# Optimization experiments

Hardware: AMD Instinct MI355X
Metric: run time of the kernel (lower is better)

## Reference

```python
import jax, jax.numpy as jnp
import numpy as np

N_GRAPHS = 32
NUM_NODES = 2848
N = N_GRAPHS * NUM_NODES  # 91136
E = 1_000_000
K = 3   # num_stacks
T = 5   # num_layers
HID = 32
EPS = 1e-5


def setup_inputs() -> dict:
    key = jax.random.key(0)
    ks = jax.random.split(key, 32)
    s = 0.1
    rn = lambda k, shp: (jax.random.normal(k, shp, jnp.float32) * s)
    inp = {
        "x": jax.random.normal(ks[0], (N, 2), jnp.float32),
        "edge_index": jax.random.randint(ks[1], (2, E), 0, N, dtype=jnp.int32).astype(jnp.int64),
        "weights": jax.random.uniform(ks[2], (E,), jnp.float32),
        "batch": (jnp.arange(N) // NUM_NODES).astype(jnp.int64),
        # ARMAConv1: 2 -> 32
        "iw1": rn(ks[3], (K, 2, HID)),
        "w1": rn(ks[4], (T - 1, K, HID, HID)),
        "rw1": rn(ks[5], (T, K, 2, HID)),
        "b1": rn(ks[6], (T, K, 1, HID)),
        "g1": jnp.ones((HID,), jnp.float32), "be1": jnp.zeros((HID,), jnp.float32),
        # ARMAConv2: 32 -> 32
        "iw2": rn(ks[7], (K, HID, HID)),
        "w2": rn(ks[8], (T - 1, K, HID, HID)),
        "rw2": rn(ks[9], (T, K, HID, HID)),
        "b2": rn(ks[10], (T, K, 1, HID)),
        "g2": jnp.ones((HID,), jnp.float32), "be2": jnp.zeros((HID,), jnp.float32),
        # ARMAConv3: 32 -> 1
        "iw3": rn(ks[11], (K, HID, 1)),
        "w3": rn(ks[12], (T - 1, K, 1, 1)),
        "rw3": rn(ks[13], (T, K, HID, 1)),
        "b3": rn(ks[14], (T, K, 1, 1)),
        "g3": jnp.ones((1,), jnp.float32), "be3": jnp.zeros((1,), jnp.float32),
        # classifier Linear(1, 1)
        "cw": rn(ks[15], (1, 1)),
        "cb": jnp.zeros((1,), jnp.float32),
    }
    return inp


def gcn_norm(row, col, w, n):
    # deg over targets, sym normalization, no self loops (PyG ARMAConv default)
    deg = jnp.zeros((n,), w.dtype).at[col].add(w)
    dis = jnp.where(deg > 0, jax.lax.rsqrt(jnp.where(deg > 0, deg, 1.0)), 0.0)
    return dis[row] * w * dis[col]


def arma_conv(x, row, col, norm, iw, w, rw, b):
    # x: [N, Fin]; returns [N, Fout] (mean over K stacks)
    out = None
    for t in range(T):
        if t == 0:
            h = jnp.einsum('nf,kfo->kno', x, iw)          # [K, N, Fout]
        else:
            h = jnp.einsum('kno,kop->knp', out, w[t - 1])
        msg = h[:, row, :] * norm[None, :, None]           # [K, E, Fout]
        agg = jnp.zeros_like(h).at[:, col, :].add(msg)     # scatter to targets
        out = jax.nn.relu(agg + jnp.einsum('nf,kfo->kno', x, rw[t]) + b[t])
    return out.mean(axis=0)


def batch_norm(x, g, b):
    m = x.mean(axis=0)
    v = x.var(axis=0)  # biased, as torch BatchNorm1d (training stats)
    return (x - m) * jax.lax.rsqrt(v + EPS) * g + b


def reference(x, edge_index, weights, batch,
              iw1, w1, rw1, b1, g1, be1,
              iw2, w2, rw2, b2, g2, be2,
              iw3, w3, rw3, b3, g3, be3,
              cw, cb):
    row, col = edge_index[0], edge_index[1]
    norm = gcn_norm(row, col, weights, N)

    h = arma_conv(x, row, col, norm, iw1, w1, rw1, b1)
    h = jax.nn.relu(batch_norm(h, g1, be1))
    h = arma_conv(h, row, col, norm, iw2, w2, rw2, b2)
    h = jax.nn.relu(batch_norm(h, g2, be2))
    h = arma_conv(h, row, col, norm, iw3, w3, rw3, b3)
    h = jax.nn.relu(batch_norm(h, g3, be3))  # [N, 1]

    # to_dense_batch: each graph has exactly NUM_NODES nodes -> reshape
    xd = h.reshape(N_GRAPHS, NUM_NODES, 1)
    logits_nodes = (xd @ cw.T + cb).squeeze(-1)   # [B, NUM_NODES]
    logits_graph = logits_nodes.max(axis=1)       # [B]
    return logits_nodes, logits_graph
```

## Files before the change

kernel.cpp:

```cpp
#include <hip/hip_runtime.h>
#include <hip/hip_fp16.h>

#define N_GRAPHS 32
#define NUM_NODES 2848
#define NTOT (N_GRAPHS * NUM_NODES)
#define NE 1000000
#define KS 3
#define TL 5
#define HID 32
#define EPSV 1e-5f
#define SCAN_B 256
#define NBLK (NTOT / SCAN_B)
#define NBINS 64
#define CNTN (NBINS * NBLK)
#define CNTB (CNTN / SCAN_B)
#define NT8 (NTOT * 8)
#define NB128 (NTOT / 128)
#define SRCMASK 0x1FFFFu

typedef unsigned uintx4 __attribute__((ext_vector_type(4)));


__device__ __forceinline__ float2 unpk(unsigned u) {
    return make_float2(__uint_as_float(u << 16), __uint_as_float(u & 0xffff0000u));
}
__device__ __forceinline__ unsigned bf16rn(float f) {
    unsigned x = __float_as_uint(f);
    return (x + 0x7fffu + ((x >> 16) & 1u)) >> 16;
}
__device__ __forceinline__ unsigned pk(float a, float b) {
    return bf16rn(a) | (bf16rn(b) << 16);
}
__device__ __forceinline__ float dec_nm(unsigned q) {
    return __half2float(__ushort_as_half((unsigned short)(q >> 17)));
}


__global__ void k_cnt(const int* __restrict__ col, int* __restrict__ indeg) {
    int e = blockIdx.x * blockDim.x + threadIdx.x;
    if (e < NE) atomicAdd(&indeg[col[e]], 1);
}

__global__ void k_lhist(const int* __restrict__ indeg, int* __restrict__ cnt) {
    __shared__ int h[NBINS];
    int t = threadIdx.x;
    if (t < NBINS) h[t] = 0;
    __syncthreads();
    int n = blockIdx.x * SCAN_B + t;
    atomicAdd(&h[min(indeg[n], NBINS - 1)], 1);
    __syncthreads();
    if (t < NBINS) cnt[t * NBLK + blockIdx.x] = h[t];
}

__global__ void k_scan1(const int* __restrict__ in, int* __restrict__ bsum) {
    __shared__ int s[SCAN_B];
    int i = blockIdx.x * SCAN_B + threadIdx.x;
    s[threadIdx.x] = in[i];
    __syncthreads();
    for (int st = SCAN_B / 2; st >= 1; st >>= 1) {
        if (threadIdx.x < st) s[threadIdx.x] += s[threadIdx.x + st];
        __syncthreads();
    }
    if (threadIdx.x == 0) bsum[blockIdx.x] = s[0];
}

__global__ void k_scan2(int* __restrict__ bsum, int n) {
    __shared__ int s[512];
    int t = threadIdx.x;
    int v = (t < n) ? bsum[t] : 0;
    s[t] = v;
    __syncthreads();
    for (int off = 1; off < 512; off <<= 1) {
        int a = (t >= off) ? s[t - off] : 0;
        __syncthreads();
        s[t] += a;
        __syncthreads();
    }
    if (t < n) bsum[t] = s[t] - v;
}

__global__ void k_scan3(const int* __restrict__ in, const int* __restrict__ bsum,
                        int* __restrict__ out, int sentIdx, int sentVal) {
    __shared__ int s[SCAN_B];
    int i = blockIdx.x * SCAN_B + threadIdx.x;
    int v = in[i];
    s[threadIdx.x] = v;
    __syncthreads();
    for (int off = 1; off < SCAN_B; off <<= 1) {
        int a = (threadIdx.x >= off) ? s[threadIdx.x - off] : 0;
        __syncthreads();
        s[threadIdx.x] += a;
        __syncthreads();
    }
    out[i] = bsum[blockIdx.x] + s[threadIdx.x] - v;
    if (i == 0 && sentIdx >= 0) out[sentIdx] = sentVal;
}

__global__ void k_rank(const int* __restrict__ indeg, const int* __restrict__ cnt,
                       int* __restrict__ perm, int* __restrict__ invperm,
                       int* __restrict__ indegp) {
    __shared__ int base[NBINS];
    __shared__ int cur[NBINS];
    int t = threadIdx.x;
    if (t < NBINS) { base[t] = cnt[t * NBLK + blockIdx.x]; cur[t] = 0; }
    __syncthreads();
    int n = blockIdx.x * SCAN_B + t;
    int dg = indeg[n];
    int b = min(dg, NBINS - 1);
    int pos = base[b] + atomicAdd(&cur[b], 1);
    perm[pos] = n;
    invperm[n] = pos;
    indegp[pos] = dg;
}

__global__ void k_xp(const float2* __restrict__ x, const int* __restrict__ perm,
                     float2* __restrict__ xp) {
    int i = blockIdx.x * blockDim.x + threadIdx.x;
    if (i < NTOT) xp[i] = x[perm[i]];
}

__global__ void k_fill(const int* __restrict__ row, const int* __restrict__ col,
                       const float* __restrict__ w, const int* __restrict__ invperm,
                       int* __restrict__ cursor, unsigned* __restrict__ adjc) {
    int e = blockIdx.x * blockDim.x + threadIdx.x;
    if (e < NE) {
        int pr = invperm[row[e]], pc = invperm[col[e]];
        int p = atomicAdd(&cursor[pc], 1);
        unsigned short hb = __half_as_ushort(__float2half(w[e]));
        adjc[p] = ((unsigned)hb << 17) | (unsigned)pr;
    }
}

__global__ void k_degdis(const unsigned* __restrict__ adjc, const int* __restrict__ offs,
                         float* __restrict__ disp) {
    int n = blockIdx.x * blockDim.x + threadIdx.x;
    if (n >= NTOT) return;
    int e0 = offs[n], e1 = offs[n + 1];
    float d = 0.f;
    for (int e = e0; e < e1; ++e) d += dec_nm(adjc[e]);
    disp[n] = (d > 0.f) ? rsqrtf(d) : 0.f;
}

__global__ void k_norm(unsigned* __restrict__ adjc, const int* __restrict__ offs,
                       const float* __restrict__ disp) {
    int n = blockIdx.x * blockDim.x + threadIdx.x;
    if (n >= NTOT) return;
    float dc = disp[n];
    int e0 = offs[n], e1 = offs[n + 1];
    for (int e = e0; e < e1; ++e) {
        unsigned q = adjc[e];
        float nm = dc * dec_nm(q) * disp[q & SRCMASK];
        unsigned short hb = __half_as_ushort(__float2half(nm));
        adjc[e] = ((unsigned)hb << 17) | (q & SRCMASK);
    }
}


__global__ __launch_bounds__(256) void k_gath(
    const unsigned* __restrict__ SRC, const int* __restrict__ offs,
    const unsigned* __restrict__ adjc, unsigned* __restrict__ P) {
    int tid = threadIdx.x;
    int u = tid & 1;
    int nl = tid >> 1;
    int bid = blockIdx.x;
    int s = bid / NB128;
    int node = (bid - s * NB128) * 128 + nl;
    const uintx4* src = (const uintx4*)(SRC + (size_t)s * NT8);
    float a0 = 0.f, a1 = 0.f, a2 = 0.f, a3 = 0.f, a4 = 0.f, a5 = 0.f, a6 = 0.f, a7 = 0.f;
    int e0 = offs[node], e1 = offs[node + 1];
    int e = e0;
    for (; e + 4 <= e1; e += 4) {
        unsigned q0 = __builtin_nontemporal_load(adjc + e);
        unsigned q1 = __builtin_nontemporal_load(adjc + e + 1);
        unsigned q2 = __builtin_nontemporal_load(adjc + e + 2);
        unsigned q3 = __builtin_nontemporal_load(adjc + e + 3);
        uintx4 v0 = src[(q0 & SRCMASK) * 2 + u];
        uintx4 v1 = src[(q1 & SRCMASK) * 2 + u];
        uintx4 v2 = src[(q2 & SRCMASK) * 2 + u];
        uintx4 v3 = src[(q3 & SRCMASK) * 2 + u];
        float n0 = dec_nm(q0), n1 = dec_nm(q1), n2 = dec_nm(q2), n3 = dec_nm(q3);
        float2 t;
        t = unpk(v0.x); a0 += n0 * t.x; a1 += n0 * t.y;
        t = unpk(v0.y); a2 += n0 * t.x; a3 += n0 * t.y;
        t = unpk(v0.z); a4 += n0 * t.x; a5 += n0 * t.y;
        t = unpk(v0.w); a6 += n0 * t.x; a7 += n0 * t.y;
        t = unpk(v1.x); a0 += n1 * t.x; a1 += n1 * t.y;
        t = unpk(v1.y); a2 += n1 * t.x; a3 += n1 * t.y;
        t = unpk(v1.z); a4 += n1 * t.x; a5 += n1 * t.y;
        t = unpk(v1.w); a6 += n1 * t.x; a7 += n1 * t.y;
        t = unpk(v2.x); a0 += n2 * t.x; a1 += n2 * t.y;
        t = unpk(v2.y); a2 += n2 * t.x; a3 += n2 * t.y;
        t = unpk(v2.z); a4 += n2 * t.x; a5 += n2 * t.y;
        t = unpk(v2.w); a6 += n2 * t.x; a7 += n2 * t.y;
        t = unpk(v3.x); a0 += n3 * t.x; a1 += n3 * t.y;
        t = unpk(v3.y); a2 += n3 * t.x; a3 += n3 * t.y;
        t = unpk(v3.z); a4 += n3 * t.x; a5 += n3 * t.y;
        t = unpk(v3.w); a6 += n3 * t.x; a7 += n3 * t.y;
    }
    for (; e < e1; ++e) {
        unsigned q0 = __builtin_nontemporal_load(adjc + e);
        uintx4 v0 = src[(q0 & SRCMASK) * 2 + u];
        float n0 = dec_nm(q0);
        float2 t;
        t = unpk(v0.x); a0 += n0 * t.x; a1 += n0 * t.y;
        t = unpk(v0.y); a2 += n0 * t.x; a3 += n0 * t.y;
        t = unpk(v0.z); a4 += n0 * t.x; a5 += n0 * t.y;
        t = unpk(v0.w); a6 += n0 * t.x; a7 += n0 * t.y;
    }
    uintx4 o;
    o.x = pk(a0, a1); o.y = pk(a2, a3); o.z = pk(a4, a5); o.w = pk(a6, a7);
    __builtin_nontemporal_store(o, (uintx4*)(P + (size_t)s * NT8 + (size_t)node * 8) + u);
}


template<int FIN, bool PERK, bool LAST>
__global__ __launch_bounds__(256) void k_xform(
    const unsigned* __restrict__ P, const float* __restrict__ xin,
    const float* __restrict__ W, const float* __restrict__ rw,
    const float* __restrict__ bb, unsigned* __restrict__ OUTn,
    float* __restrict__ xm) {
    constexpr int SPK = PERK ? 3 : 1;
    constexpr int NSEC = PERK ? 6 : 2;
    constexpr int ND = 128;
    __shared__ unsigned sp[SPK][ND][17];
    __shared__ float xr[FIN == 32 ? ND : 1][FIN == 32 ? 33 : 1];
    int tid = threadIdx.x;
    int node0 = blockIdx.x * ND;
    for (int t4 = tid; t4 < NSEC * 256; t4 += 256) {
        int s = t4 >> 8, r = t4 & 255, n = r >> 1, u4 = (r & 1) * 4;
        uintx4 v = *(const uintx4*)(P + (size_t)s * NT8 + (size_t)(node0 + n) * 8 + u4);
        int kk = PERK ? (s >> 1) : 0;
        int base = (s & 1) * 8 + u4;
        sp[kk][n][base]     = v.x;
        sp[kk][n][base + 1] = v.y;
        sp[kk][n][base + 2] = v.z;
        sp[kk][n][base + 3] = v.w;
    }
    if constexpr (FIN == 32) {
        for (int t4 = tid; t4 < ND * 8; t4 += 256) {
            int n = t4 >> 3, j4 = (t4 & 7) * 4;
            float4 v = ((const float4*)xin)[(size_t)(node0 + n) * 8 + (t4 & 7)];
            xr[n][j4] = v.x; xr[n][j4 + 1] = v.y; xr[n][j4 + 2] = v.z; xr[n][j4 + 3] = v.w;
        }
    }
    __syncthreads();
    int f2 = tid & 15, nl = tid >> 4;
    int nbase = nl * 8;
    float2 xv2[8];
    if constexpr (FIN == 2) {
#pragma unroll
        for (int n = 0; n < 8; ++n) xv2[n] = ((const float2*)xin)[node0 + nbase + n];
    }
    float m0[8] = {}, m1[8] = {};
#pragma unroll
    for (int k = 0; k < KS; ++k) {
        constexpr int kkI = 0;
        const int kk = PERK ? k : kkI;
        float2 bv = ((const float2*)(bb + k * HID))[f2];
        float h0[8], h1[8];
#pragma unroll
        for (int n = 0; n < 8; ++n) { h0[n] = bv.x; h1[n] = bv.y; }
        const float2* W2 = (const float2*)(W + (size_t)k * HID * HID);
        const float2* R2 = (const float2*)(rw + (size_t)k * FIN * HID);
#pragma unroll 4
        for (int i2 = 0; i2 < 16; ++i2) {
            float2 wf0 = W2[(2 * i2) * 16 + f2];
            float2 wf1 = W2[(2 * i2 + 1) * 16 + f2];
            float2 rf0, rf1;
            if constexpr (FIN == 32) {
                rf0 = R2[(2 * i2) * 16 + f2];
                rf1 = R2[(2 * i2 + 1) * 16 + f2];
            }
#pragma unroll
            for (int n = 0; n < 8; ++n) {
                float2 sv = unpk(sp[kk][nbase + n][i2]);
                h0[n] += sv.x * wf0.x + sv.y * wf1.x;
                h1[n] += sv.x * wf0.y + sv.y * wf1.y;
                if constexpr (FIN == 32) {
                    float x0 = xr[nbase + n][2 * i2], x1 = xr[nbase + n][2 * i2 + 1];
                    h0[n] += x0 * rf0.x + x1 * rf1.x;
                    h1[n] += x0 * rf0.y + x1 * rf1.y;
                }
            }
        }
        if constexpr (FIN == 2) {
            float2 r0 = R2[0 * 16 + f2], r1 = R2[1 * 16 + f2];
#pragma unroll
            for (int n = 0; n < 8; ++n) {
                h0[n] += xv2[n].x * r0.x + xv2[n].y * r1.x;
                h1[n] += xv2[n].x * r0.y + xv2[n].y * r1.y;
            }
        }
#pragma unroll
        for (int n = 0; n < 8; ++n) {
            h0[n] = fmaxf(h0[n], 0.f);
            h1[n] = fmaxf(h1[n], 0.f);
            if constexpr (LAST) {
                m0[n] += h0[n]; m1[n] += h1[n];
            } else {
                OUTn[(size_t)(k * 2 + (f2 >> 3)) * NT8 +
                     (size_t)(node0 + nbase + n) * 8 + (f2 & 7)] = pk(h0[n], h1[n]);
            }
        }
    }
    if constexpr (LAST) {
#pragma unroll
        for (int n = 0; n < 8; ++n)
            ((float2*)xm)[(size_t)(node0 + nbase + n) * 16 + f2] =
                make_float2(m0[n] * (1.f / 3.f), m1[n] * (1.f / 3.f));
    }
}


__global__ void k_gath2(const float2* __restrict__ xp, const int* __restrict__ offs,
                        const unsigned* __restrict__ adjc, float2* __restrict__ pag) {
    int node = blockIdx.x * blockDim.x + threadIdx.x;
    if (node >= NTOT) return;
    float a0 = 0.f, a1 = 0.f;
    int e0 = offs[node], e1 = offs[node + 1];
    int e = e0;
    for (; e + 4 <= e1; e += 4) {
        unsigned q0 = __builtin_nontemporal_load(adjc + e);
        unsigned q1 = __builtin_nontemporal_load(adjc + e + 1);
        unsigned q2 = __builtin_nontemporal_load(adjc + e + 2);
        unsigned q3 = __builtin_nontemporal_load(adjc + e + 3);
        float2 x0 = xp[q0 & SRCMASK], x1 = xp[q1 & SRCMASK];
        float2 x2 = xp[q2 & SRCMASK], x3 = xp[q3 & SRCMASK];
        float n0 = dec_nm(q0), n1 = dec_nm(q1), n2 = dec_nm(q2), n3 = dec_nm(q3);
        a0 += n0 * x0.x + n1 * x1.x + n2 * x2.x + n3 * x3.x;
        a1 += n0 * x0.y + n1 * x1.y + n2 * x2.y + n3 * x3.y;
    }
    for (; e < e1; ++e) {
        unsigned q0 = __builtin_nontemporal_load(adjc + e);
        float2 xs = xp[q0 & SRCMASK];
        float nm = dec_nm(q0);
        a0 += nm * xs.x; a1 += nm * xs.y;
    }
    pag[node] = make_float2(a0, a1);
}

__global__ void k_x0(const float2* __restrict__ pag, const float2* __restrict__ xp,
                     const float* __restrict__ iw, const float* __restrict__ rw0,
                     const float* __restrict__ b0, unsigned* __restrict__ OUT) {
    int tid = blockIdx.x * blockDim.x + threadIdx.x;
    int f2 = tid & 15;
    int node = tid >> 4;
    float2 pv = pag[node];
    float2 xn = xp[node];
#pragma unroll
    for (int k = 0; k < KS; ++k) {
        const float2* iw2 = (const float2*)(iw + k * 2 * HID);
        const float2* rw2 = (const float2*)(rw0 + k * 2 * HID);
        float2 wi0 = iw2[0 * 16 + f2], wi1 = iw2[1 * 16 + f2];
        float2 wr0 = rw2[0 * 16 + f2], wr1 = rw2[1 * 16 + f2];
        float2 bv = ((const float2*)(b0 + k * HID))[f2];
        float o0 = fmaxf(pv.x * wi0.x + pv.y * wi1.x + xn.x * wr0.x + xn.y * wr1.x + bv.x, 0.f);
        float o1 = fmaxf(pv.x * wi0.y + pv.y * wi1.y + xn.x * wr0.y + xn.y * wr1.y + bv.y, 0.f);
        OUT[(size_t)(k * 2 + (f2 >> 3)) * NT8 + (size_t)node * 8 + (f2 & 7)] = pk(o0, o1);
    }
}


__global__ void k_rec3(const float* __restrict__ xb, const float* __restrict__ iw3,
                       const float* __restrict__ rw3, const float* __restrict__ b3,
                       float4* __restrict__ H0, float4* __restrict__ RT) {
    int n = blockIdx.x * blockDim.x + threadIdx.x;
    if (n >= NTOT) return;
    float xr[HID];
#pragma unroll
    for (int j = 0; j < 8; ++j) {
        float4 v = ((const float4*)xb)[(size_t)n * 8 + j];
        xr[4 * j] = v.x; xr[4 * j + 1] = v.y; xr[4 * j + 2] = v.z; xr[4 * j + 3] = v.w;
    }
    {
        float a0 = 0.f, a1 = 0.f, a2 = 0.f;
#pragma unroll
        for (int i = 0; i < HID; ++i) {
            a0 += xr[i] * iw3[0 * HID + i];
            a1 += xr[i] * iw3[1 * HID + i];
            a2 += xr[i] * iw3[2 * HID + i];
        }
        H0[n] = make_float4(a0, a1, a2, 0.f);
    }
#pragma unroll
    for (int t = 0; t < TL; ++t) {
        float a0 = b3[t * KS + 0], a1 = b3[t * KS + 1], a2 = b3[t * KS + 2];
        const float* r = rw3 + (size_t)t * KS * HID;
#pragma unroll
        for (int i = 0; i < HID; ++i) {
            a0 += xr[i] * r[0 * HID + i];
            a1 += xr[i] * r[1 * HID + i];
            a2 += xr[i] * r[2 * HID + i];
        }
        RT[(size_t)t * NTOT + n] = make_float4(a0, a1, a2, 0.f);
    }
}

template<bool LAST>
__global__ void k_prop1(const float4* __restrict__ H, const float4* __restrict__ RT,
                        const float* __restrict__ W_t, const int* __restrict__ offs,
                        const unsigned* __restrict__ adjc, const int* __restrict__ perm,
                        float* __restrict__ outp) {
    int node = blockIdx.x * blockDim.x + threadIdx.x;
    if (node >= NTOT) return;
    float4 rt = RT[node];
    float a0 = rt.x, a1 = rt.y, a2 = rt.z;
    int e0 = offs[node], e1 = offs[node + 1];
    int e = e0;
    for (; e + 4 <= e1; e += 4) {
        unsigned q0 = __builtin_nontemporal_load(adjc + e);
        unsigned q1 = __builtin_nontemporal_load(adjc + e + 1);
        unsigned q2 = __builtin_nontemporal_load(adjc + e + 2);
        unsigned q3 = __builtin_nontemporal_load(adjc + e + 3);
        float4 h0 = H[q0 & SRCMASK], h1 = H[q1 & SRCMASK];
        float4 h2 = H[q2 & SRCMASK], h3 = H[q3 & SRCMASK];
        float n0 = dec_nm(q0), n1 = dec_nm(q1), n2 = dec_nm(q2), n3 = dec_nm(q3);
        a0 += n0 * h0.x; a1 += n0 * h0.y; a2 += n0 * h0.z;
        a0 += n1 * h1.x; a1 += n1 * h1.y; a2 += n1 * h1.z;
        a0 += n2 * h2.x; a1 += n2 * h2.y; a2 += n2 * h2.z;
        a0 += n3 * h3.x; a1 += n3 * h3.y; a2 += n3 * h3.z;
    }
    for (; e < e1; ++e) {
        unsigned q0 = __builtin_nontemporal_load(adjc + e);
        float4 h = H[q0 & SRCMASK];
        float nm = dec_nm(q0);
        a0 += nm * h.x; a1 += nm * h.y; a2 += nm * h.z;
    }
    a0 = fmaxf(a0, 0.f); a1 = fmaxf(a1, 0.f); a2 = fmaxf(a2, 0.f);
    if constexpr (LAST) {
        outp[perm[node]] = (a0 + a1 + a2) * (1.f / 3.f);
    } else {
        ((float4*)outp)[node] = make_float4(a0 * W_t[0], a1 * W_t[1], a2 * W_t[2], 0.f);
    }
}


__global__ void k_bnstats(const float* __restrict__ x, float* __restrict__ stats, int F) {
    __shared__ float s1[256];
    __shared__ float s2[256];
    int tid = threadIdx.x;
    int gid = blockIdx.x * blockDim.x + tid;
    int stride = gridDim.x * blockDim.x;
    int total = NTOT * F;
    float a = 0.f, b = 0.f;
    for (int i = gid; i < total; i += stride) {
        float v = x[i];
        a += v;
        b += v * v;
    }
    s1[tid] = a; s2[tid] = b;
    __syncthreads();
    for (int s = 128; s >= F; s >>= 1) {
        if (tid < s) { s1[tid] += s1[tid + s]; s2[tid] += s2[tid + s]; }
        __syncthreads();
    }
    if (tid < F) {
        atomicAdd(&stats[tid], s1[tid]);
        atomicAdd(&stats[F + tid], s2[tid]);
    }
}

__global__ void k_bnapply32(float* __restrict__ x, const float* __restrict__ stats,
                            const float* __restrict__ g, const float* __restrict__ be,
                            unsigned* __restrict__ xbf) {
    int tid = blockIdx.x * blockDim.x + threadIdx.x;
    int f2 = tid & 15;
    int node = tid >> 4;
    int f0 = 2 * f2, f1 = f0 + 1;
    float mm0 = stats[f0] * (1.f / NTOT);
    float vv0 = stats[HID + f0] * (1.f / NTOT) - mm0 * mm0;
    float mm1 = stats[f1] * (1.f / NTOT);
    float vv1 = stats[HID + f1] * (1.f / NTOT) - mm1 * mm1;
    float y0 = fmaxf((x[(size_t)node * 32 + f0] - mm0) * rsqrtf(vv0 + EPSV) * g[f0] + be[f0], 0.f);
    float y1 = fmaxf((x[(size_t)node * 32 + f1] - mm1) * rsqrtf(vv1 + EPSV) * g[f1] + be[f1], 0.f);
    x[(size_t)node * 32 + f0] = y0;
    x[(size_t)node * 32 + f1] = y1;
    if (xbf) xbf[(size_t)(f2 >> 3) * NT8 + (size_t)node * 8 + (f2 & 7)] = pk(y0, y1);
}

__global__ void k_bnapply1(float* __restrict__ x, const float* __restrict__ stats,
                           const float* __restrict__ g, const float* __restrict__ be) {
    int i = blockIdx.x * blockDim.x + threadIdx.x;
    if (i >= NTOT) return;
    float m = stats[0] * (1.f / NTOT);
    float v = stats[1] * (1.f / NTOT) - m * m;
    float y = (x[i] - m) * rsqrtf(v + EPSV) * g[0] + be[0];
    x[i] = fmaxf(y, 0.f);
}


__global__ void k_final(const float* __restrict__ h, const float* __restrict__ cw,
                        const float* __restrict__ cb, float* __restrict__ out) {
    __shared__ float smax[256];
    int g = blockIdx.x;
    float cwv = cw[0], cbv = cb[0];
    float mx = -INFINITY;
    for (int i = threadIdx.x; i < NUM_NODES; i += blockDim.x) {
        int nidx = g * NUM_NODES + i;
        float v = h[nidx] * cwv + cbv;
        out[nidx] = v;
        mx = fmaxf(mx, v);
    }
    smax[threadIdx.x] = mx;
    __syncthreads();
    for (int s = 128; s >= 1; s >>= 1) {
        if (threadIdx.x < s) smax[threadIdx.x] = fmaxf(smax[threadIdx.x], smax[threadIdx.x + s]);
        __syncthreads();
    }
    if (threadIdx.x == 0) out[NTOT + g] = smax[0];
}


extern "C" void kernel_launch(void* const* d_in, const int* in_sizes, int n_in,
                              void* d_out, int out_size, void* d_ws, size_t ws_size,
                              hipStream_t stream) {
    const float* x   = (const float*)d_in[0];
    const int*   ei  = (const int*)d_in[1];
    const int*   row = ei;
    const int*   col = ei + NE;
    const float* wts = (const float*)d_in[2];
    const float* iw1 = (const float*)d_in[4];
    const float* w1  = (const float*)d_in[5];
    const float* rw1 = (const float*)d_in[6];
    const float* b1  = (const float*)d_in[7];
    const float* g1  = (const float*)d_in[8];
    const float* be1 = (const float*)d_in[9];
    const float* iw2 = (const float*)d_in[10];
    const float* w2  = (const float*)d_in[11];
    const float* rw2 = (const float*)d_in[12];
    const float* b2  = (const float*)d_in[13];
    const float* g2  = (const float*)d_in[14];
    const float* be2 = (const float*)d_in[15];
    const float* iw3 = (const float*)d_in[16];
    const float* w3  = (const float*)d_in[17];
    const float* rw3 = (const float*)d_in[18];
    const float* b3  = (const float*)d_in[19];
    const float* g3  = (const float*)d_in[20];
    const float* be3 = (const float*)d_in[21];
    const float* cw  = (const float*)d_in[22];
    const float* cb  = (const float*)d_in[23];
    float* out = (float*)d_out;

    char* p = (char*)d_ws;
    auto alloc = [&](size_t bytes) {
        char* r = p;
        p += (bytes + 255) & ~(size_t)255;
        return r;
    };
    int*      indeg  = (int*)alloc((size_t)NTOT * 4);
    int*      cnt    = (int*)alloc((size_t)CNTN * 4);
    char*     zend   = p;
    int*      bsum   = (int*)alloc((size_t)NBLK * 4);
    int*      offs   = (int*)alloc((size_t)(NTOT + 1) * 4);
    int*      cursor = (int*)alloc((size_t)NTOT * 4);
    int*      perm   = (int*)alloc((size_t)NTOT * 4);
    int*      invperm= (int*)alloc((size_t)NTOT * 4);
    int*      indegp = (int*)alloc((size_t)NTOT * 4);
    float*    disp   = (float*)alloc((size_t)NTOT * 4);
    unsigned* adjc   = (unsigned*)alloc((size_t)NE * 4);
    unsigned* OUTA   = (unsigned*)alloc((size_t)6 * NT8 * 4);
    unsigned* OUTB   = (unsigned*)alloc((size_t)6 * NT8 * 4);
    unsigned* P      = (unsigned*)alloc((size_t)6 * NT8 * 4);
    unsigned* xplane = (unsigned*)alloc((size_t)2 * NT8 * 4);
    float2*   xp     = (float2*)alloc((size_t)NTOT * 8);
    float2*   pag    = (float2*)alloc((size_t)NTOT * 8);
    float*    xa     = (float*)alloc((size_t)NTOT * HID * 4);
    float*    xb     = (float*)alloc((size_t)NTOT * HID * 4);
    float*    xc     = (float*)alloc((size_t)NTOT * 4);
    float4*   RT     = (float4*)alloc((size_t)TL * NTOT * 16);
    float*    stats  = (float*)alloc(3 * 2 * HID * 4);
    if ((size_t)(p - (char*)d_ws) > ws_size) return;

    const int tb = 256;
    const int ebl = (NE + tb - 1) / tb;
    const int nbl = NTOT / tb;
    const int g16 = NTOT * 16 / tb;

    hipMemsetAsync(indeg, 0, (size_t)(zend - (char*)indeg), stream);
    hipMemsetAsync(stats, 0, (size_t)3 * 2 * HID * 4, stream);

    k_cnt<<<ebl, tb, 0, stream>>>(col, indeg);
    k_lhist<<<NBLK, SCAN_B, 0, stream>>>(indeg, cnt);
    k_scan1<<<CNTB, SCAN_B, 0, stream>>>(cnt, bsum);
    k_scan2<<<1, 512, 0, stream>>>(bsum, CNTB);
    k_scan3<<<CNTB, SCAN_B, 0, stream>>>(cnt, bsum, cnt, -1, 0);
    k_rank<<<NBLK, SCAN_B, 0, stream>>>(indeg, cnt, perm, invperm, indegp);
    k_xp<<<nbl, tb, 0, stream>>>((const float2*)x, perm, xp);
    k_scan1<<<NBLK, SCAN_B, 0, stream>>>(indegp, bsum);
    k_scan2<<<1, 512, 0, stream>>>(bsum, NBLK);
    k_scan3<<<NBLK, SCAN_B, 0, stream>>>(indegp, bsum, offs, NTOT, NE);
    hipMemcpyAsync(cursor, offs, (size_t)NTOT * 4, hipMemcpyDeviceToDevice, stream);
    k_fill<<<ebl, tb, 0, stream>>>(row, col, wts, invperm, cursor, adjc);
    k_degdis<<<nbl, tb, 0, stream>>>(adjc, offs, disp);
    k_norm<<<nbl, tb, 0, stream>>>(adjc, offs, disp);

    {
        k_gath2<<<nbl, tb, 0, stream>>>(xp, offs, adjc, pag);
        k_x0<<<g16, tb, 0, stream>>>(pag, xp, iw1, rw1, b1, OUTA);
        unsigned* Hc = OUTA; unsigned* Hn = OUTB;
        for (int t = 1; t < TL - 1; ++t) {
            k_gath<<<6 * NB128, tb, 0, stream>>>(Hc, offs, adjc, P);
            k_xform<2, true, false><<<NB128, tb, 0, stream>>>(
                P, (const float*)xp, w1 + (size_t)(t - 1) * KS * HID * HID,
                rw1 + (size_t)t * KS * 2 * HID, b1 + (size_t)t * KS * HID, Hn, nullptr);
            unsigned* tmp = Hc; Hc = Hn; Hn = tmp;
        }
        k_gath<<<6 * NB128, tb, 0, stream>>>(Hc, offs, adjc, P);
        k_xform<2, true, true><<<NB128, tb, 0, stream>>>(
            P, (const float*)xp, w1 + (size_t)(TL - 2) * KS * HID * HID,
            rw1 + (size_t)(TL - 1) * KS * 2 * HID, b1 + (size_t)(TL - 1) * KS * HID,
            nullptr, xa);
        k_bnstats<<<256, tb, 0, stream>>>(xa, stats, HID);
        k_bnapply32<<<g16, tb, 0, stream>>>(xa, stats, g1, be1, xplane);
    }
    {
        k_gath<<<2 * NB128, tb, 0, stream>>>(xplane, offs, adjc, P);
        k_xform<32, false, false><<<NB128, tb, 0, stream>>>(
            P, xa, iw2, rw2, b2, OUTA, nullptr);
        unsigned* Hc = OUTA; unsigned* Hn = OUTB;
        for (int t = 1; t < TL - 1; ++t) {
            k_gath<<<6 * NB128, tb, 0, stream>>>(Hc, offs, adjc, P);
            k_xform<32, true, false><<<NB128, tb, 0, stream>>>(
                P, xa, w2 + (size_t)(t - 1) * KS * HID * HID,
                rw2 + (size_t)t * KS * HID * HID, b2 + (size_t)t * KS * HID, Hn, nullptr);
            unsigned* tmp = Hc; Hc = Hn; Hn = tmp;
        }
        k_gath<<<6 * NB128, tb, 0, stream>>>(Hc, offs, adjc, P);
        k_xform<32, true, true><<<NB128, tb, 0, stream>>>(
            P, xa, w2 + (size_t)(TL - 2) * KS * HID * HID,
            rw2 + (size_t)(TL - 1) * KS * HID * HID, b2 + (size_t)(TL - 1) * KS * HID,
            nullptr, xb);
        k_bnstats<<<256, tb, 0, stream>>>(xb, stats + 2 * HID, HID);
        k_bnapply32<<<g16, tb, 0, stream>>>(xb, stats + 2 * HID, g2, be2, nullptr);
    }
    {
        float4* HAf = (float4*)OUTA;
        float4* HBf = (float4*)OUTB;
        k_rec3<<<nbl, tb, 0, stream>>>(xb, iw3, rw3, b3, HAf, RT);
        const float4* Hc = HAf; float4* Hn = HBf;
        for (int t = 0; t < TL - 1; ++t) {
            k_prop1<false><<<nbl, tb, 0, stream>>>(
                Hc, RT + (size_t)t * NTOT, w3 + (size_t)t * KS, offs, adjc, perm, (float*)Hn);
            const float4* tmp = Hc; Hc = Hn; Hn = (float4*)tmp;
        }
        k_prop1<true><<<nbl, tb, 0, stream>>>(
            Hc, RT + (size_t)(TL - 1) * NTOT, nullptr, offs, adjc, perm, xc);
        k_bnstats<<<256, tb, 0, stream>>>(xc, stats + 4 * HID, 1);
        k_bnapply1<<<nbl, tb, 0, stream>>>(xc, stats + 4 * HID, g3, be3);
    }

    k_final<<<N_GRAPHS, 256, 0, stream>>>(xc, cw, cb, out);
}
```

Before: 1.166 ms.

## Fuse BN stats into final xform, stage outputs via LDS, split degree atomics

```diff
diff --git a/kernel.cpp b/kernel.cpp
--- a/kernel.cpp
+++ b/kernel.cpp
@@ -36,9 +36,17 @@
 }
 
 
-__global__ void k_cnt(const int* __restrict__ col, int* __restrict__ indeg) {
+__global__ void k_cnt(const int* __restrict__ col, int* __restrict__ indegS) {
     int e = blockIdx.x * blockDim.x + threadIdx.x;
-    if (e < NE) atomicAdd(&indeg[col[e]], 1);
+    if (e < NE) atomicAdd(&indegS[(col[e] << 2) | (e & 3)], 1);
+}
+
+__global__ void k_merge(const int* __restrict__ indegS, int* __restrict__ indeg) {
+    int n = blockIdx.x * blockDim.x + threadIdx.x;
+    if (n < NTOT) {
+        int4 v = ((const int4*)indegS)[n];
+        indeg[n] = v.x + v.y + v.z + v.w;
+    }
 }
 
 __global__ void k_lhist(const int* __restrict__ indeg, int* __restrict__ cnt) {
@@ -218,11 +226,10 @@
     const unsigned* __restrict__ P, const float* __restrict__ xin,
     const float* __restrict__ W, const float* __restrict__ rw,
     const float* __restrict__ bb, unsigned* __restrict__ OUTn,
-    float* __restrict__ xm) {
-    constexpr int SPK = PERK ? 3 : 1;
+    float* __restrict__ xm, float* __restrict__ stats) {
     constexpr int NSEC = PERK ? 6 : 2;
     constexpr int ND = 128;
-    __shared__ unsigned sp[SPK][ND][17];
+    __shared__ unsigned sp[KS][ND][17];
     __shared__ float xr[FIN == 32 ? ND : 1][FIN == 32 ? 33 : 1];
     int tid = threadIdx.x;
     int node0 = blockIdx.x * ND;
@@ -252,10 +259,10 @@
         for (int n = 0; n < 8; ++n) xv2[n] = ((const float2*)xin)[node0 + nbase + n];
     }
     float m0[8] = {}, m1[8] = {};
+    unsigned uo[KS][8];
 #pragma unroll
     for (int k = 0; k < KS; ++k) {
-        constexpr int kkI = 0;
-        const int kk = PERK ? k : kkI;
+        const int kk = PERK ? k : 0;
         float2 bv = ((const float2*)(bb + k * HID))[f2];
         float h0[8], h1[8];
 #pragma unroll
@@ -298,16 +305,59 @@
             if constexpr (LAST) {
                 m0[n] += h0[n]; m1[n] += h1[n];
             } else {
-                OUTn[(size_t)(k * 2 + (f2 >> 3)) * NT8 +
-                     (size_t)(node0 + nbase + n) * 8 + (f2 & 7)] = pk(h0[n], h1[n]);
+                uo[k][n] = pk(h0[n], h1[n]);
             }
         }
     }
     if constexpr (LAST) {
-#pragma unroll
-        for (int n = 0; n < 8; ++n)
-            ((float2*)xm)[(size_t)(node0 + nbase + n) * 16 + f2] =
-                make_float2(m0[n] * (1.f / 3.f), m1[n] * (1.f / 3.f));
+        float sv0 = 0.f, sq0 = 0.f, sv1 = 0.f, sq1 = 0.f;
+#pragma unroll
+        for (int n = 0; n < 8; ++n) {
+            float v0 = m0[n] * (1.f / 3.f), v1 = m1[n] * (1.f / 3.f);
+            ((float2*)xm)[(size_t)(node0 + nbase + n) * 16 + f2] = make_float2(v0, v1);
+            sv0 += v0; sq0 += v0 * v0;
+            sv1 += v1; sq1 += v1 * v1;
+        }
+        float* red = (float*)sp;
+        __syncthreads();
+        red[0 * 256 + f2 * 16 + nl] = sv0;
+        red[1 * 256 + f2 * 16 + nl] = sq0;
+        red[2 * 256 + f2 * 16 + nl] = sv1;
+        red[3 * 256 + f2 * 16 + nl] = sq1;
+        __syncthreads();
+        if (nl == 0) {
+            float a = 0.f, b = 0.f, c = 0.f, d = 0.f;
+#pragma unroll
+            for (int j = 0; j < 16; ++j) {
+                a += red[0 * 256 + f2 * 16 + j];
+                b += red[1 * 256 + f2 * 16 + j];
+                c += red[2 * 256 + f2 * 16 + j];
+                d += red[3 * 256 + f2 * 16 + j];
+            }
+            atomicAdd(&stats[2 * f2], a);
+            atomicAdd(&stats[HID + 2 * f2], b);
+            atomicAdd(&stats[2 * f2 + 1], c);
+            atomicAdd(&stats[HID + 2 * f2 + 1], d);
+        }
+    } else {
+#pragma unroll
+        for (int k = 0; k < KS; ++k)
+#pragma unroll
+            for (int n = 0; n < 8; ++n)
+                sp[k][nbase + n][f2] = uo[k][n];
+        __syncthreads();
+        for (int t4 = tid; t4 < 6 * 256; t4 += 256) {
+            int s = t4 >> 8, r = t4 & 255, n = r >> 1, u4 = (r & 1) * 4;
+            int kk = s >> 1;
+            int base = (s & 1) * 8 + u4;
+            uintx4 v;
+            v.x = sp[kk][n][base];
+            v.y = sp[kk][n][base + 1];
+            v.z = sp[kk][n][base + 2];
+            v.w = sp[kk][n][base + 3];
+            __builtin_nontemporal_store(
+                v, (uintx4*)(OUTn + (size_t)s * NT8 + (size_t)(node0 + n) * 8 + u4));
+        }
     }
 }
 
@@ -547,9 +597,11 @@
         p += (bytes + 255) & ~(size_t)255;
         return r;
     };
+    int*      indegS = (int*)alloc((size_t)NTOT * 16);
+    int*      cnt    = (int*)alloc((size_t)CNTN * 4);
+    float*    stats  = (float*)alloc(3 * 2 * HID * 4);
+    char*     zend   = p;
     int*      indeg  = (int*)alloc((size_t)NTOT * 4);
-    int*      cnt    = (int*)alloc((size_t)CNTN * 4);
-    char*     zend   = p;
     int*      bsum   = (int*)alloc((size_t)NBLK * 4);
     int*      offs   = (int*)alloc((size_t)(NTOT + 1) * 4);
     int*      cursor = (int*)alloc((size_t)NTOT * 4);
@@ -568,7 +620,6 @@
     float*    xb     = (float*)alloc((size_t)NTOT * HID * 4);
     float*    xc     = (float*)alloc((size_t)NTOT * 4);
     float4*   RT     = (float4*)alloc((size_t)TL * NTOT * 16);
-    float*    stats  = (float*)alloc(3 * 2 * HID * 4);
     if ((size_t)(p - (char*)d_ws) > ws_size) return;
 
     const int tb = 256;
@@ -576,10 +627,10 @@
     const int nbl = NTOT / tb;
     const int g16 = NTOT * 16 / tb;
 
-    hipMemsetAsync(indeg, 0, (size_t)(zend - (char*)indeg), stream);
-    hipMemsetAsync(stats, 0, (size_t)3 * 2 * HID * 4, stream);
-
-    k_cnt<<<ebl, tb, 0, stream>>>(col, indeg);
+    hipMemsetAsync(indegS, 0, (size_t)(zend - (char*)indegS), stream);
+
+    k_cnt<<<ebl, tb, 0, stream>>>(col, indegS);
+    k_merge<<<nbl, tb, 0, stream>>>(indegS, indeg);
     k_lhist<<<NBLK, SCAN_B, 0, stream>>>(indeg, cnt);
     k_scan1<<<CNTB, SCAN_B, 0, stream>>>(cnt, bsum);
     k_scan2<<<1, 512, 0, stream>>>(bsum, CNTB);
@@ -602,35 +653,35 @@
             k_gath<<<6 * NB128, tb, 0, stream>>>(Hc, offs, adjc, P);
             k_xform<2, true, false><<<NB128, tb, 0, stream>>>(
                 P, (const float*)xp, w1 + (size_t)(t - 1) * KS * HID * HID,
-                rw1 + (size_t)t * KS * 2 * HID, b1 + (size_t)t * KS * HID, Hn, nullptr);
+                rw1 + (size_t)t * KS * 2 * HID, b1 + (size_t)t * KS * HID, Hn,
+                nullptr, nullptr);
             unsigned* tmp = Hc; Hc = Hn; Hn = tmp;
         }
         k_gath<<<6 * NB128, tb, 0, stream>>>(Hc, offs, adjc, P);
         k_xform<2, true, true><<<NB128, tb, 0, stream>>>(
             P, (const float*)xp, w1 + (size_t)(TL - 2) * KS * HID * HID,
             rw1 + (size_t)(TL - 1) * KS * 2 * HID, b1 + (size_t)(TL - 1) * KS * HID,
-            nullptr, xa);
-        k_bnstats<<<256, tb, 0, stream>>>(xa, stats, HID);
+            nullptr, xa, stats);
         k_bnapply32<<<g16, tb, 0, stream>>>(xa, stats, g1, be1, xplane);
     }
     {
         k_gath<<<2 * NB128, tb, 0, stream>>>(xplane, offs, adjc, P);
         k_xform<32, false, false><<<NB128, tb, 0, stream>>>(
-            P, xa, iw2, rw2, b2, OUTA, nullptr);
+            P, xa, iw2, rw2, b2, OUTA, nullptr, nullptr);
         unsigned* Hc = OUTA; unsigned* Hn = OUTB;
         for (int t = 1; t < TL - 1; ++t) {
             k_gath<<<6 * NB128, tb, 0, stream>>>(Hc, offs, adjc, P);
             k_xform<32, true, false><<<NB128, tb, 0, stream>>>(
                 P, xa, w2 + (size_t)(t - 1) * KS * HID * HID,
-                rw2 + (size_t)t * KS * HID * HID, b2 + (size_t)t * KS * HID, Hn, nullptr);
+                rw2 + (size_t)t * KS * HID * HID, b2 + (size_t)t * KS * HID, Hn,
+                nullptr, nullptr);
             unsigned* tmp = Hc; Hc = Hn; Hn = tmp;
         }
         k_gath<<<6 * NB128, tb, 0, stream>>>(Hc, offs, adjc, P);
         k_xform<32, true, true><<<NB128, tb, 0, stream>>>(
             P, xa, w2 + (size_t)(TL - 2) * KS * HID * HID,
             rw2 + (size_t)(TL - 1) * KS * HID * HID, b2 + (size_t)(TL - 1) * KS * HID,
-            nullptr, xb);
-        k_bnstats<<<256, tb, 0, stream>>>(xb, stats + 2 * HID, HID);
+            nullptr, xb, stats + 2 * HID);
         k_bnapply32<<<g16, tb, 0, stream>>>(xb, stats + 2 * HID, g2, be2, nullptr);
     }
     {
```

New measurement: 1.177 ms. No clear change (+1.0%).

## Split xform across stacks, fuse mean with BN stats, spread degree atomics

Applied to the files above, without the earlier changes.

```diff
diff --git a/kernel.cpp b/kernel.cpp
--- a/kernel.cpp
+++ b/kernel.cpp
@@ -36,9 +36,17 @@
 }
 
 
-__global__ void k_cnt(const int* __restrict__ col, int* __restrict__ indeg) {
+__global__ void k_cnt(const int* __restrict__ col, int* __restrict__ indegS) {
     int e = blockIdx.x * blockDim.x + threadIdx.x;
-    if (e < NE) atomicAdd(&indeg[col[e]], 1);
+    if (e < NE) atomicAdd(&indegS[(col[e] << 2) | (e & 3)], 1);
+}
+
+__global__ void k_merge(const int* __restrict__ indegS, int* __restrict__ indeg) {
+    int n = blockIdx.x * blockDim.x + threadIdx.x;
+    if (n < NTOT) {
+        int4 v = ((const int4*)indegS)[n];
+        indeg[n] = v.x + v.y + v.z + v.w;
+    }
 }
 
 __global__ void k_lhist(const int* __restrict__ indeg, int* __restrict__ cnt) {
@@ -213,101 +221,124 @@
 }
 
 
-template<int FIN, bool PERK, bool LAST>
-__global__ __launch_bounds__(256) void k_xform(
+template<int FIN, bool SHARED, bool LAST>
+__global__ __launch_bounds__(256) void k_xformk(
     const unsigned* __restrict__ P, const float* __restrict__ xin,
     const float* __restrict__ W, const float* __restrict__ rw,
-    const float* __restrict__ bb, unsigned* __restrict__ OUTn,
-    float* __restrict__ xm) {
-    constexpr int SPK = PERK ? 3 : 1;
-    constexpr int NSEC = PERK ? 6 : 2;
-    constexpr int ND = 128;
-    __shared__ unsigned sp[SPK][ND][17];
-    __shared__ float xr[FIN == 32 ? ND : 1][FIN == 32 ? 33 : 1];
+    const float* __restrict__ bb, void* __restrict__ outp) {
+    __shared__ float sp[128][33];
+    __shared__ unsigned xr[FIN == 32 ? 128 : 1][FIN == 32 ? 17 : 1];
     int tid = threadIdx.x;
-    int node0 = blockIdx.x * ND;
-    for (int t4 = tid; t4 < NSEC * 256; t4 += 256) {
-        int s = t4 >> 8, r = t4 & 255, n = r >> 1, u4 = (r & 1) * 4;
-        uintx4 v = *(const uintx4*)(P + (size_t)s * NT8 + (size_t)(node0 + n) * 8 + u4);
-        int kk = PERK ? (s >> 1) : 0;
-        int base = (s & 1) * 8 + u4;
-        sp[kk][n][base]     = v.x;
-        sp[kk][n][base + 1] = v.y;
-        sp[kk][n][base + 2] = v.z;
-        sp[kk][n][base + 3] = v.w;
+    int bid = blockIdx.x;
+    int k = bid / NB128;
+    int node0 = (bid - k * NB128) * 128;
+    int sbase = SHARED ? 0 : k * 2;
+
+    for (int t4 = tid; t4 < 512; t4 += 256) {
+        int s2 = t4 >> 8, r = t4 & 255, n = r >> 1, u4 = (r & 1) * 4;
+        uintx4 v = *(const uintx4*)(P + (size_t)(sbase + s2) * NT8 +
+                                    (size_t)(node0 + n) * 8 + u4);
+        int base = s2 * 16 + u4 * 2;
+        float2 t;
+        t = unpk(v.x); sp[n][base]     = t.x; sp[n][base + 1] = t.y;
+        t = unpk(v.y); sp[n][base + 2] = t.x; sp[n][base + 3] = t.y;
+        t = unpk(v.z); sp[n][base + 4] = t.x; sp[n][base + 5] = t.y;
+        t = unpk(v.w); sp[n][base + 6] = t.x; sp[n][base + 7] = t.y;
     }
     if constexpr (FIN == 32) {
-        for (int t4 = tid; t4 < ND * 8; t4 += 256) {
-            int n = t4 >> 3, j4 = (t4 & 7) * 4;
-            float4 v = ((const float4*)xin)[(size_t)(node0 + n) * 8 + (t4 & 7)];
-            xr[n][j4] = v.x; xr[n][j4 + 1] = v.y; xr[n][j4 + 2] = v.z; xr[n][j4 + 3] = v.w;
-        }
-    }
-    __syncthreads();
+        for (int t4 = tid; t4 < 128 * 8; t4 += 256) {
+            int n = t4 >> 3, j = t4 & 7;
+            float4 v = ((const float4*)xin)[(size_t)(node0 + n) * 8 + j];
+            xr[n][2 * j]     = pk(v.x, v.y);
+            xr[n][2 * j + 1] = pk(v.z, v.w);
+        }
+    }
+    __syncthreads();
+
     int f2 = tid & 15, nl = tid >> 4;
     int nbase = nl * 8;
-    float2 xv2[8];
+    float2 xv2[FIN == 2 ? 8 : 1];
     if constexpr (FIN == 2) {
 #pragma unroll
         for (int n = 0; n < 8; ++n) xv2[n] = ((const float2*)xin)[node0 + nbase + n];
     }
-    float m0[8] = {}, m1[8] = {};
-#pragma unroll
-    for (int k = 0; k < KS; ++k) {
-        constexpr int kkI = 0;
-        const int kk = PERK ? k : kkI;
-        float2 bv = ((const float2*)(bb + k * HID))[f2];
-        float h0[8], h1[8];
-#pragma unroll
-        for (int n = 0; n < 8; ++n) { h0[n] = bv.x; h1[n] = bv.y; }
-        const float2* W2 = (const float2*)(W + (size_t)k * HID * HID);
-        const float2* R2 = (const float2*)(rw + (size_t)k * FIN * HID);
+    const float2* W2 = (const float2*)(W + (size_t)k * HID * HID);
+    const float2* R2 = (const float2*)(rw + (size_t)k * FIN * HID);
+    float2 bv = ((const float2*)(bb + k * HID))[f2];
+    float h0[8], h1[8];
+#pragma unroll
+    for (int n = 0; n < 8; ++n) { h0[n] = bv.x; h1[n] = bv.y; }
+
 #pragma unroll 4
-        for (int i2 = 0; i2 < 16; ++i2) {
-            float2 wf0 = W2[(2 * i2) * 16 + f2];
-            float2 wf1 = W2[(2 * i2 + 1) * 16 + f2];
-            float2 rf0, rf1;
+    for (int i2 = 0; i2 < 16; ++i2) {
+        float2 wf0 = W2[(2 * i2) * 16 + f2];
+        float2 wf1 = W2[(2 * i2 + 1) * 16 + f2];
+        float2 rf0, rf1;
+        if constexpr (FIN == 32) {
+            rf0 = R2[(2 * i2) * 16 + f2];
+            rf1 = R2[(2 * i2 + 1) * 16 + f2];
+        }
+#pragma unroll
+        for (int n = 0; n < 8; ++n) {
+            float s0 = sp[nbase + n][2 * i2];
+            float s1 = sp[nbase + n][2 * i2 + 1];
+            h0[n] += s0 * wf0.x + s1 * wf1.x;
+            h1[n] += s0 * wf0.y + s1 * wf1.y;
             if constexpr (FIN == 32) {
-                rf0 = R2[(2 * i2) * 16 + f2];
-                rf1 = R2[(2 * i2 + 1) * 16 + f2];
+                float2 xq = unpk(xr[nbase + n][i2]);
+                h0[n] += xq.x * rf0.x + xq.y * rf1.x;
+                h1[n] += xq.x * rf0.y + xq.y * rf1.y;
             }
-#pragma unroll
-            for (int n = 0; n < 8; ++n) {
-                float2 sv = unpk(sp[kk][nbase + n][i2]);
-                h0[n] += sv.x * wf0.x + sv.y * wf1.x;
-                h1[n] += sv.x * wf0.y + sv.y * wf1.y;
-                if constexpr (FIN == 32) {
-                    float x0 = xr[nbase + n][2 * i2], x1 = xr[nbase + n][2 * i2 + 1];
-                    h0[n] += x0 * rf0.x + x1 * rf1.x;
-                    h1[n] += x0 * rf0.y + x1 * rf1.y;
-                }
-            }
-        }
-        if constexpr (FIN == 2) {
-            float2 r0 = R2[0 * 16 + f2], r1 = R2[1 * 16 + f2];
-#pragma unroll
-            for (int n = 0; n < 8; ++n) {
-                h0[n] += xv2[n].x * r0.x + xv2[n].y * r1.x;
-                h1[n] += xv2[n].x * r0.y + xv2[n].y * r1.y;
-            }
-        }
+        }
+    }
+    if constexpr (FIN == 2) {
+        float2 r0 = R2[0 * 16 + f2], r1 = R2[1 * 16 + f2];
 #pragma unroll
         for (int n = 0; n < 8; ++n) {
-            h0[n] = fmaxf(h0[n], 0.f);
-            h1[n] = fmaxf(h1[n], 0.f);
-            if constexpr (LAST) {
-                m0[n] += h0[n]; m1[n] += h1[n];
-            } else {
-                OUTn[(size_t)(k * 2 + (f2 >> 3)) * NT8 +
-                     (size_t)(node0 + nbase + n) * 8 + (f2 & 7)] = pk(h0[n], h1[n]);
-            }
-        }
-    }
+            h0[n] += xv2[n].x * r0.x + xv2[n].y * r1.x;
+            h1[n] += xv2[n].x * r0.y + xv2[n].y * r1.y;
+        }
+    }
+
     if constexpr (LAST) {
+        float2* xo = (float2*)outp + (size_t)k * (NTOT * 16);
 #pragma unroll
         for (int n = 0; n < 8; ++n)
-            ((float2*)xm)[(size_t)(node0 + nbase + n) * 16 + f2] =
-                make_float2(m0[n] * (1.f / 3.f), m1[n] * (1.f / 3.f));
+            xo[(size_t)(node0 + nbase + n) * 16 + f2] =
+                make_float2(fmaxf(h0[n], 0.f), fmaxf(h1[n], 0.f));
+    } else {
+        unsigned* O = (unsigned*)outp;
+#pragma unroll
+        for (int n = 0; n < 8; ++n)
+            O[(size_t)(k * 2 + (f2 >> 3)) * NT8 + (size_t)(node0 + nbase + n) * 8 +
+              (f2 & 7)] = pk(fmaxf(h0[n], 0.f), fmaxf(h1[n], 0.f));
+    }
+}
+
+__global__ void k_meanstats(const float* __restrict__ x0, const float* __restrict__ x1,
+                            const float* __restrict__ x2, float* __restrict__ xm,
+                            float* __restrict__ stats) {
+    __shared__ float s1[256];
+    __shared__ float s2[256];
+    int tid = threadIdx.x;
+    int gid = blockIdx.x * blockDim.x + tid;
+    int stride = gridDim.x * blockDim.x;
+    float a = 0.f, b = 0.f;
+    for (int i = gid; i < NTOT * HID; i += stride) {
+        float v = (x0[i] + x1[i] + x2[i]) * (1.f / 3.f);
+        xm[i] = v;
+        a += v;
+        b += v * v;
+    }
+    s1[tid] = a; s2[tid] = b;
+    __syncthreads();
+    for (int s = 128; s >= HID; s >>= 1) {
+        if (tid < s) { s1[tid] += s1[tid + s]; s2[tid] += s2[tid + s]; }
+        __syncthreads();
+    }
+    if (tid < HID) {
+        atomicAdd(&stats[tid], s1[tid]);
+        atomicAdd(&stats[HID + tid], s2[tid]);
     }
 }
 
@@ -547,9 +578,11 @@
         p += (bytes + 255) & ~(size_t)255;
         return r;
     };
+    int*      indegS = (int*)alloc((size_t)NTOT * 16);
+    int*      cnt    = (int*)alloc((size_t)CNTN * 4);
+    float*    stats  = (float*)alloc(3 * 2 * HID * 4);
+    char*     zend   = p;
     int*      indeg  = (int*)alloc((size_t)NTOT * 4);
-    int*      cnt    = (int*)alloc((size_t)CNTN * 4);
-    char*     zend   = p;
     int*      bsum   = (int*)alloc((size_t)NBLK * 4);
     int*      offs   = (int*)alloc((size_t)(NTOT + 1) * 4);
     int*      cursor = (int*)alloc((size_t)NTOT * 4);
@@ -568,18 +601,19 @@
     float*    xb     = (float*)alloc((size_t)NTOT * HID * 4);
     float*    xc     = (float*)alloc((size_t)NTOT * 4);
     float4*   RT     = (float4*)alloc((size_t)TL * NTOT * 16);
-    float*    stats  = (float*)alloc(3 * 2 * HID * 4);
     if ((size_t)(p - (char*)d_ws) > ws_size) return;
+
+    float* xo = (float*)OUTA;
 
     const int tb = 256;
     const int ebl = (NE + tb - 1) / tb;
     const int nbl = NTOT / tb;
     const int g16 = NTOT * 16 / tb;
 
-    hipMemsetAsync(indeg, 0, (size_t)(zend - (char*)indeg), stream);
-    hipMemsetAsync(stats, 0, (size_t)3 * 2 * HID * 4, stream);
-
-    k_cnt<<<ebl, tb, 0, stream>>>(col, indeg);
+    hipMemsetAsync(indegS, 0, (size_t)(zend - (char*)indegS), stream);
+
+    k_cnt<<<ebl, tb, 0, stream>>>(col, indegS);
+    k_merge<<<nbl, tb, 0, stream>>>(indegS, indeg);
     k_lhist<<<NBLK, SCAN_B, 0, stream>>>(indeg, cnt);
     k_scan1<<<CNTB, SCAN_B, 0, stream>>>(cnt, bsum);
     k_scan2<<<1, 512, 0, stream>>>(bsum, CNTB);
@@ -600,37 +634,37 @@
         unsigned* Hc = OUTA; unsigned* Hn = OUTB;
         for (int t = 1; t < TL - 1; ++t) {
             k_gath<<<6 * NB128, tb, 0, stream>>>(Hc, offs, adjc, P);
-            k_xform<2, true, false><<<NB128, tb, 0, stream>>>(
+            k_xformk<2, false, false><<<3 * NB128, tb, 0, stream>>>(
                 P, (const float*)xp, w1 + (size_t)(t - 1) * KS * HID * HID,
-                rw1 + (size_t)t * KS * 2 * HID, b1 + (size_t)t * KS * HID, Hn, nullptr);
+                rw1 + (size_t)t * KS * 2 * HID, b1 + (size_t)t * KS * HID, Hn);
             unsigned* tmp = Hc; Hc = Hn; Hn = tmp;
         }
         k_gath<<<6 * NB128, tb, 0, stream>>>(Hc, offs, adjc, P);
-        k_xform<2, true, true><<<NB128, tb, 0, stream>>>(
+        k_xformk<2, false, true><<<3 * NB128, tb, 0, stream>>>(
             P, (const float*)xp, w1 + (size_t)(TL - 2) * KS * HID * HID,
-            rw1 + (size_t)(TL - 1) * KS * 2 * HID, b1 + (size_t)(TL - 1) * KS * HID,
-            nullptr, xa);
-        k_bnstats<<<256, tb, 0, stream>>>(xa, stats, HID);
+            rw1 + (size_t)(TL - 1) * KS * 2 * HID, b1 + (size_t)(TL - 1) * KS * HID, xo);
+        k_meanstats<<<256, tb, 0, stream>>>(xo, xo + (size_t)NTOT * HID,
+                                            xo + (size_t)2 * NTOT * HID, xa, stats);
         k_bnapply32<<<g16, tb, 0, stream>>>(xa, stats, g1, be1, xplane);
     }
     {
         k_gath<<<2 * NB128, tb, 0, stream>>>(xplane, offs, adjc, P);
-        k_xform<32, false, false><<<NB128, tb, 0, stream>>>(
-            P, xa, iw2, rw2, b2, OUTA, nullptr);
+        k_xformk<32, true, false><<<3 * NB128, tb, 0, stream>>>(
+            P, xa, iw2, rw2, b2, OUTA);
         unsigned* Hc = OUTA; unsigned* Hn = OUTB;
         for (int t = 1; t < TL - 1; ++t) {
             k_gath<<<6 * NB128, tb, 0, stream>>>(Hc, offs, adjc, P);
-            k_xform<32, true, false><<<NB128, tb, 0, stream>>>(
+            k_xformk<32, false, false><<<3 * NB128, tb, 0, stream>>>(
                 P, xa, w2 + (size_t)(t - 1) * KS * HID * HID,
-                rw2 + (size_t)t * KS * HID * HID, b2 + (size_t)t * KS * HID, Hn, nullptr);
+                rw2 + (size_t)t * KS * HID * HID, b2 + (size_t)t * KS * HID, Hn);
             unsigned* tmp = Hc; Hc = Hn; Hn = tmp;
         }
         k_gath<<<6 * NB128, tb, 0, stream>>>(Hc, offs, adjc, P);
-        k_xform<32, true, true><<<NB128, tb, 0, stream>>>(
+        k_xformk<32, false, true><<<3 * NB128, tb, 0, stream>>>(
             P, xa, w2 + (size_t)(TL - 2) * KS * HID * HID,
-            rw2 + (size_t)(TL - 1) * KS * HID * HID, b2 + (size_t)(TL - 1) * KS * HID,
-            nullptr, xb);
-        k_bnstats<<<256, tb, 0, stream>>>(xb, stats + 2 * HID, HID);
+            rw2 + (size_t)(TL - 1) * KS * HID * HID, b2 + (size_t)(TL - 1) * KS * HID, xo);
+        k_meanstats<<<256, tb, 0, stream>>>(xo, xo + (size_t)NTOT * HID,
+                                            xo + (size_t)2 * NTOT * HID, xb, stats + 2 * HID);
         k_bnapply32<<<g16, tb, 0, stream>>>(xb, stats + 2 * HID, g2, be2, nullptr);
     }
     {
```

Result: faster. 1.120 ms (-3.9%).
